# Optimization experiments

Measured on AMD Instinct MI355X. Metric: run time of the kernel, lower is better.

Reference implementation:

```python
import jax, jax.numpy as jnp
import numpy as np

N = 50000      # nodes
E = 640000     # edges
D_IN = 128     # input_dimension
H = 128        # hidden_dimension
D_OUT = 64     # output_dimension
G = 500        # num graphs
L = 2          # gnn layers (conv->norm->act stages each)
TEMP = 1.0     # mic_archi_param_temperature
EPS = 1e-5


def setup_inputs() -> dict:
    key = jax.random.key(0)
    ks = jax.random.split(key, 20)
    s = 1.0 / np.sqrt(H)
    inp = {
        "x": jax.random.normal(ks[0], (N, D_IN), jnp.float32),
        "edge_index": jax.random.randint(ks[1], (2, E), 0, N, dtype=jnp.int64),
        "batch": jnp.sort(jax.random.randint(ks[2], (N,), 0, G, dtype=jnp.int64)),
        # pre/post process MLPs (single Linear each)
        "pre_w": jax.random.normal(ks[3], (D_IN, H), jnp.float32) * s,
        "pre_b": jnp.zeros((H,), jnp.float32),
        "post_w": jax.random.normal(ks[4], (H, D_OUT), jnp.float32) * s,
        "post_b": jnp.zeros((D_OUT,), jnp.float32),
        # per-layer conv candidates: GCNConv + SAGEConv (stacked over L layers)
        "gcn_w": jax.random.normal(ks[5], (L, H, H), jnp.float32) * s,
        "gcn_b": jnp.zeros((L, H), jnp.float32),
        "sage_ws": jax.random.normal(ks[6], (L, H, H), jnp.float32) * s,
        "sage_wn": jax.random.normal(ks[7], (L, H, H), jnp.float32) * s,
        # per-layer norm candidate params (LayerNorm; Identity has none)
        "ln_g": jnp.ones((L, H), jnp.float32),
        "ln_b": jnp.zeros((L, H), jnp.float32),
        # architecture parameters (uniform init as in the torch code)
        "a_conv": jax.random.uniform(ks[8], (L, 2), jnp.float32),
        "a_norm": jax.random.uniform(ks[9], (L, 2), jnp.float32),
        "a_act": jax.random.uniform(ks[10], (L, 3), jnp.float32),
    }
    return inp


def reference(x, edge_index, batch, pre_w, pre_b, post_w, post_b,
              gcn_w, gcn_b, sage_ws, sage_wn, ln_g, ln_b,
              a_conv, a_norm, a_act):
    src, dst = edge_index[0], edge_index[1]
    loop = jnp.arange(N, dtype=src.dtype)
    # GCN uses self-loops + symmetric normalization
    src_sl = jnp.concatenate([src, loop])
    dst_sl = jnp.concatenate([dst, loop])
    deg = jax.ops.segment_sum(jnp.ones((E + N,), jnp.float32), dst_sl, num_segments=N)
    dinv = jax.lax.rsqrt(deg)  # deg >= 1 due to self-loops
    gcn_norm = (dinv[src_sl] * dinv[dst_sl])[:, None]  # [E+N, 1]
    # SAGE mean aggregation (no self loops)
    deg_n = jnp.clip(jax.ops.segment_sum(jnp.ones((E,), jnp.float32), dst, num_segments=N), 1.0)

    def gcn(h, w, b):
        hw = h @ w  # [N, H]
        agg = jax.ops.segment_sum(hw[src_sl] * gcn_norm, dst_sl, num_segments=N)
        return agg + b

    def sage(h, ws, wn):
        mean = jax.ops.segment_sum(h[src], dst, num_segments=N) / deg_n[:, None]
        return h @ ws + mean @ wn

    def layernorm(h, g, b):
        mu = jnp.mean(h, axis=-1, keepdims=True)
        var = jnp.mean(jnp.square(h - mu), axis=-1, keepdims=True)
        return (h - mu) * jax.lax.rsqrt(var + EPS) * g + b

    h = x @ pre_w + pre_b  # pre-process MLP
    layer_outputs = []
    for l in range(L):
        wc = jax.nn.softmax(a_conv[l] / TEMP)
        h = wc[0] * gcn(h, gcn_w[l], gcn_b[l]) + wc[1] * sage(h, sage_ws[l], sage_wn[l])
        wn_ = jax.nn.softmax(a_norm[l] / TEMP)
        h = wn_[0] * layernorm(h, ln_g[l], ln_b[l]) + wn_[1] * h
        wa = jax.nn.softmax(a_act[l] / TEMP)
        h = wa[0] * jax.nn.relu(h) + wa[1] * jnp.tanh(h) + wa[2] * jax.nn.elu(h)
        layer_outputs.append(h)  # collected after each act stage (skip connections)

    skip = layer_outputs[0]
    for o in layer_outputs[1:]:
        skip = skip + o
    pooled = jax.ops.segment_sum(skip, batch, num_segments=G)  # sum pooling readout
    return pooled @ post_w + post_b
```

## Files before the change

### kernel.cpp

```cpp
#include <hip/hip_runtime.h>
#include <hip/hip_fp16.h>
#include <math.h>

#define N_NODES 50000
#define N_EDGES 640000
#define HDIM    128
#define D_OUT   64
#define G_GRAPHS 500
#define EPSV    1e-5f
#define WPM     16384
#define CAP     64
#define SENT    N_NODES
#define NSHARD  8
#define SHARD_SZ ((N_NODES + NSHARD - 1) / NSHARD)

typedef __bf16 v8bf __attribute__((ext_vector_type(8)));
typedef float  f32x4 __attribute__((ext_vector_type(4)));

static __device__ __forceinline__ float bf_lo(unsigned u) {
    union { unsigned x; float f; } c; c.x = u << 16; return c.f;
}
static __device__ __forceinline__ float bf_hi(unsigned u) {
    union { unsigned x; float f; } c; c.x = u & 0xffff0000u; return c.f;
}

__global__ void setup_kernel(const float* __restrict__ pre_w,
                             const float* __restrict__ gcn_w,
                             const float* __restrict__ sws,
                             const float* __restrict__ swn,
                             const float* __restrict__ a_conv,
                             __bf16* __restrict__ Wp,
                             int* __restrict__ cnt,
                             float* __restrict__ pooled,
                             uint4* __restrict__ csr4,
                             uint4* __restrict__ hrow0,
                             uint4* __restrict__ hrow1)
{
    int t = blockIdx.x * blockDim.x + threadIdx.x;
    const unsigned sv = ((unsigned)SENT << 16) | (unsigned)SENT;
    if (t < N_NODES * CAP / 8) csr4[t] = make_uint4(sv, sv, sv, sv);
    if (t < N_NODES) cnt[t] = 0;
    if (t < G_GRAPHS * 128) pooled[t] = 0.f;
    if (t < 16) {
        hrow0[t] = make_uint4(0, 0, 0, 0);
        hrow1[t] = make_uint4(0, 0, 0, 0);
    }
    if (t >= 7 * 2048) return;
    int m    = t >> 11;
    int r    = t & 2047;
    int lane = r & 63;
    int fb   = r >> 6;
    int kc   = fb >> 3;
    int cb   = fb & 7;
    const float* W = pre_w;
    float scale = 1.f;
    if (m > 0) {
        int type = (m - 1) >> 1;
        int l    = (m - 1) & 1;
        float c0 = a_conv[l * 2], c1 = a_conv[l * 2 + 1];
        float mx = fmaxf(c0, c1);
        float e0 = __expf(c0 - mx), e1 = __expf(c1 - mx);
        float wc0 = e0 / (e0 + e1);
        scale = (type == 0) ? wc0 : (1.f - wc0);
        W = (type == 0) ? gcn_w + (size_t)l * WPM
          : (type == 1) ? sws   + (size_t)l * WPM
                        : swn   + (size_t)l * WPM;
    }
    int k0  = kc * 32 + (lane >> 4) * 8;
    int col = cb * 16 + (lane & 15);
    __bf16* out = Wp + (size_t)m * WPM + ((size_t)fb * 64 + lane) * 8;
    #pragma unroll
    for (int i = 0; i < 8; i++)
        out[i] = (__bf16)(scale * W[(size_t)(k0 + i) * 128 + col]);
}

__global__ void csr_fill_kernel(const int* __restrict__ src, const int* __restrict__ dst,
                                int* __restrict__ cnt,
                                unsigned short* __restrict__ csr, int E) {
    int chunk = blockIdx.x >> 3;
    int shard = blockIdx.x & 7;
    int e = chunk * 256 + threadIdx.x;
    if (e >= E) return;
    int d = dst[e];
    if (d / SHARD_SZ != shard) return;
    int s = src[e];
    int pos = atomicAdd(&cnt[d], 1);
    csr[(d << 6) + pos] = (unsigned short)s;
}

__global__ void dinvh_kernel(const int* __restrict__ cnt, __half* __restrict__ dinvh, int n) {
    int i = blockIdx.x * blockDim.x + threadIdx.x;
    if (i < n)  dinvh[i] = __float2half(rsqrtf((float)cnt[i] + 1.0f));
    if (i == n) dinvh[i] = __float2half(0.f);
}

__global__ __launch_bounds__(256) void fused_gather_bf16(
    const __bf16* __restrict__ hb,
    const unsigned short* __restrict__ csr,
    const int* __restrict__ cnt,
    const __half* __restrict__ dinvh,
    __bf16* __restrict__ aggGb,
    __bf16* __restrict__ meanb, int n)
{
    int w = threadIdx.x >> 6;
    int lane = threadIdx.x & 63;
    int d = blockIdx.x * 4 + w;
    if (d >= n) return;
    int c = cnt[d];
    float cf = (float)c;
    float did = rsqrtf(cf + 1.0f);
    float rd  = 1.0f / fmaxf(cf, 1.0f);
    int base = d << 6;
    int iters = (c + 15) >> 4;
    int q  = lane >> 4;
    int c8 = (lane & 15) * 8;

    float aG[8] = {0, 0, 0, 0, 0, 0, 0, 0};
    float aS[8] = {0, 0, 0, 0, 0, 0, 0, 0};

    for (int p = 0; p < iters; p++) {
        int s[4];
        #pragma unroll
        for (int k = 0; k < 4; k++)
            s[k] = csr[base + p * 16 + 4 * k + q];
        uint4 u[4];
        float ds[4];
        #pragma unroll
        for (int k = 0; k < 4; k++) {
            u[k]  = *(const uint4*)(hb + (size_t)s[k] * 128 + c8);
            ds[k] = __half2float(dinvh[s[k]]);
        }
        #pragma unroll
        for (int k = 0; k < 4; k++) {
            float wk = ds[k] * did;
            float v[8] = { bf_lo(u[k].x), bf_hi(u[k].x), bf_lo(u[k].y), bf_hi(u[k].y),
                           bf_lo(u[k].z), bf_hi(u[k].z), bf_lo(u[k].w), bf_hi(u[k].w) };
            #pragma unroll
            for (int j = 0; j < 8; j++) {
                aG[j] = fmaf(v[j], wk, aG[j]);
                aS[j] += v[j];
            }
        }
    }
    #pragma unroll
    for (int j = 0; j < 8; j++) {
        aG[j] += __shfl_xor(aG[j], 16);
        aG[j] += __shfl_xor(aG[j], 32);
        aS[j] += __shfl_xor(aS[j], 16);
        aS[j] += __shfl_xor(aS[j], 32);
    }
    if (q == 0) {
        uint4 ud = *(const uint4*)(hb + (size_t)d * 128 + c8);
        float vd[8] = { bf_lo(ud.x), bf_hi(ud.x), bf_lo(ud.y), bf_hi(ud.y),
                        bf_lo(ud.z), bf_hi(ud.z), bf_lo(ud.w), bf_hi(ud.w) };
        float sl = did * did;
        union { __bf16 b[8]; uint4 u; } pg, pm;
        #pragma unroll
        for (int j = 0; j < 8; j++) {
            pg.b[j] = (__bf16)fmaf(vd[j], sl, aG[j]);
            pm.b[j] = (__bf16)(aS[j] * rd);
        }
        *(uint4*)(aggGb + (size_t)d * 128 + c8) = pg.u;
        *(uint4*)(meanb + (size_t)d * 128 + c8) = pm.u;
    }
}

__global__ __launch_bounds__(256) void pre_gemm_mfma(
    const float* __restrict__ x, const __bf16* __restrict__ Wp0,
    const float* __restrict__ pre_b, __bf16* __restrict__ hb, int n)
{
    __shared__ __bf16 wlds[WPM];
    const int tid  = threadIdx.x;
    const int w    = tid >> 6;
    const int lane = tid & 63;
    const int r0 = blockIdx.x * 64 + w * 16;
    int rl = r0 + (lane & 15);
    if (rl >= n) rl = n - 1;
    const int kg = lane >> 4;

    {
        uint4* lds4 = (uint4*)wlds;
        const uint4* g = (const uint4*)Wp0;
        #pragma unroll
        for (int it = 0; it < 8; it++)
            lds4[it * 256 + tid] = g[it * 256 + tid];
    }

    f32x4 acc[8];
    #pragma unroll
    for (int cb = 0; cb < 8; cb++) acc[cb] = (f32x4)(0.f);

    v8bf af[4];
    #pragma unroll
    for (int kc = 0; kc < 4; kc++) {
        const float* ap = x + (size_t)rl * 128 + kc * 32 + kg * 8;
        float4 a0 = *(const float4*)ap;
        float4 a1 = *(const float4*)(ap + 4);
        v8bf v;
        v[0] = (__bf16)a0.x; v[1] = (__bf16)a0.y;
        v[2] = (__bf16)a0.z; v[3] = (__bf16)a0.w;
        v[4] = (__bf16)a1.x; v[5] = (__bf16)a1.y;
        v[6] = (__bf16)a1.z; v[7] = (__bf16)a1.w;
        af[kc] = v;
    }
    __syncthreads();

    #pragma unroll
    for (int kc = 0; kc < 4; kc++) {
        #pragma unroll
        for (int cb = 0; cb < 8; cb++) {
            int bo = ((kc * 8 + cb) * 64 + lane) * 8;
            acc[cb] = __builtin_amdgcn_mfma_f32_16x16x32_bf16(
                af[kc], *(const v8bf*)&wlds[bo], acc[cb], 0, 0, 0);
        }
    }
    int cl = lane & 15;
    #pragma unroll
    for (int cb = 0; cb < 8; cb++) {
        float bias = pre_b[cb * 16 + cl];
        #pragma unroll
        for (int j = 0; j < 4; j++) {
            int r = r0 + kg * 4 + j;
            if (r < n) hb[(size_t)r * 128 + cb * 16 + cl] = (__bf16)(acc[cb][j] + bias);
        }
    }
}

__global__ __launch_bounds__(256, 3) void layer_gemm_kernel(
    const __bf16* __restrict__ aggGb, const __bf16* __restrict__ hin,
    const __bf16* __restrict__ meanb,
    const __bf16* __restrict__ WpG, const __bf16* __restrict__ WpS,
    const __bf16* __restrict__ WpN,
    const float* __restrict__ gcn_b,
    const float* __restrict__ lng, const float* __restrict__ lnb,
    const float* __restrict__ anorm, const float* __restrict__ aact,
    const float* __restrict__ aconv,
    __bf16* __restrict__ hout, int n)
{
    __shared__ __bf16 wlds[3 * 16 * 64 * 8];
    const int tid  = threadIdx.x;
    const int w    = tid >> 6;
    const int lane = tid & 63;
    const int r0 = blockIdx.x * 64 + w * 16;
    int rl = r0 + (lane & 15);
    if (rl >= n) rl = n - 1;
    const int kg = lane >> 4;

    v8bf af[12];
    #pragma unroll
    for (int kc = 0; kc < 4; kc++) {
        size_t ao = (size_t)rl * 128 + kc * 32 + kg * 8;
        af[kc]     = *(const v8bf*)(aggGb + ao);
        af[4 + kc] = *(const v8bf*)(hin   + ao);
        af[8 + kc] = *(const v8bf*)(meanb + ao);
    }

    f32x4 acc[8];
    #pragma unroll
    for (int cb = 0; cb < 8; cb++) acc[cb] = (f32x4)(0.f);

    uint4* lds4 = (uint4*)wlds;

    {
        const uint4* gG = (const uint4*)WpG;
        const uint4* gS = (const uint4*)WpS;
        const uint4* gN = (const uint4*)WpN;
        #pragma unroll
        for (int it = 0; it < 12; it++) {
            int idx = it * 256 + tid;
            int m = idx >> 10;
            int r = idx & 1023;
            const uint4* g = (m == 0) ? gG : (m == 1) ? gS : gN;
            lds4[idx] = g[r];
        }
    }
    __syncthreads();
    #pragma unroll
    for (int kc2 = 0; kc2 < 2; kc2++) {
        #pragma unroll
        for (int cb = 0; cb < 8; cb++) {
            int bo = ((kc2 * 8 + cb) * 64 + lane) * 8;
            acc[cb] = __builtin_amdgcn_mfma_f32_16x16x32_bf16(
                af[kc2], *(const v8bf*)&wlds[bo], acc[cb], 0, 0, 0);
            acc[cb] = __builtin_amdgcn_mfma_f32_16x16x32_bf16(
                af[4 + kc2], *(const v8bf*)&wlds[8192 + bo], acc[cb], 0, 0, 0);
            acc[cb] = __builtin_amdgcn_mfma_f32_16x16x32_bf16(
                af[8 + kc2], *(const v8bf*)&wlds[16384 + bo], acc[cb], 0, 0, 0);
        }
    }
    __syncthreads();

    {
        const uint4* gG = (const uint4*)WpG + 1024;
        const uint4* gS = (const uint4*)WpS + 1024;
        const uint4* gN = (const uint4*)WpN + 1024;
        #pragma unroll
        for (int it = 0; it < 12; it++) {
            int idx = it * 256 + tid;
            int m = idx >> 10;
            int r = idx & 1023;
            const uint4* g = (m == 0) ? gG : (m == 1) ? gS : gN;
            lds4[idx] = g[r];
        }
    }
    __syncthreads();
    #pragma unroll
    for (int kc2 = 0; kc2 < 2; kc2++) {
        #pragma unroll
        for (int cb = 0; cb < 8; cb++) {
            int bo = ((kc2 * 8 + cb) * 64 + lane) * 8;
            acc[cb] = __builtin_amdgcn_mfma_f32_16x16x32_bf16(
                af[2 + kc2], *(const v8bf*)&wlds[bo], acc[cb], 0, 0, 0);
            acc[cb] = __builtin_amdgcn_mfma_f32_16x16x32_bf16(
                af[6 + kc2], *(const v8bf*)&wlds[8192 + bo], acc[cb], 0, 0, 0);
            acc[cb] = __builtin_amdgcn_mfma_f32_16x16x32_bf16(
                af[10 + kc2], *(const v8bf*)&wlds[16384 + bo], acc[cb], 0, 0, 0);
        }
    }

    float c0 = aconv[0], c1 = aconv[1];
    float m = fmaxf(c0, c1);
    float e0 = __expf(c0 - m), e1 = __expf(c1 - m);
    float wc0 = e0 / (e0 + e1);
    float q0 = anorm[0], q1 = anorm[1];
    m = fmaxf(q0, q1);
    e0 = __expf(q0 - m); e1 = __expf(q1 - m);
    float wn0 = e0 / (e0 + e1), wn1 = 1.f - wn0;
    float a0 = aact[0], a1 = aact[1], a2 = aact[2];
    m = fmaxf(fmaxf(a0, a1), a2);
    float f0 = __expf(a0 - m), f1 = __expf(a1 - m), f2 = __expf(a2 - m);
    float fs = 1.f / (f0 + f1 + f2);
    float wa0 = f0 * fs, wa1 = f1 * fs, wa2 = f2 * fs;

    int cl = lane & 15;
    float gbF[8], lg[8], lb[8];
    #pragma unroll
    for (int cb = 0; cb < 8; cb++) {
        int c = cb * 16 + cl;
        gbF[cb] = wc0 * gcn_b[c]; lg[cb] = lng[c]; lb[cb] = lnb[c];
    }

    float s[4] = {0, 0, 0, 0}, s2[4] = {0, 0, 0, 0};
    #pragma unroll
    for (int cb = 0; cb < 8; cb++)
        #pragma unroll
        for (int j = 0; j < 4; j++) {
            float tv = acc[cb][j] + gbF[cb];
            acc[cb][j] = tv;
            s[j] += tv;
            s2[j] = fmaf(tv, tv, s2[j]);
        }
    #pragma unroll
    for (int o = 1; o < 16; o <<= 1)
        #pragma unroll
        for (int j = 0; j < 4; j++) {
            s[j]  += __shfl_xor(s[j], o);
            s2[j] += __shfl_xor(s2[j], o);
        }
    float mu[4], rs[4];
    #pragma unroll
    for (int j = 0; j < 4; j++) {
        mu[j] = s[j] * (1.f / 128.f);
        float var = s2[j] * (1.f / 128.f) - mu[j] * mu[j];
        rs[j] = rsqrtf(var + EPSV);
    }

    #pragma unroll
    for (int j = 0; j < 4; j++) {
        int r = r0 + kg * 4 + j;
        if (r >= n) continue;
        #pragma unroll
        for (int cb = 0; cb < 8; cb++) {
            float tv = acc[cb][j];
            float ln = (tv - mu[j]) * rs[j] * lg[cb] + lb[cb];
            float hv = wn0 * ln + wn1 * tv;
            float rl_ = fmaxf(hv, 0.f);
            float ex2 = __expf(2.f * hv);
            float th = 1.f - 2.f * __builtin_amdgcn_rcpf(ex2 + 1.f);
            float el = hv > 0.f ? hv : __expf(hv) - 1.f;
            float out = wa0 * rl_ + wa1 * th + wa2 * el;
            hout[(size_t)r * 128 + cb * 16 + cl] = (__bf16)out;
        }
    }
}

__global__ __launch_bounds__(256) void pool_sum_kernel(
    const __bf16* __restrict__ h1, const __bf16* __restrict__ h2,
    const int* __restrict__ batch, float* __restrict__ pooled, int n)
{
    int c2  = (threadIdx.x & 63) * 2;
    int seg = threadIdx.x >> 6;
    int n0  = blockIdx.x * 128 + seg * 32;
    int g_cur = -1;
    float acc0 = 0.f, acc1 = 0.f;
    for (int i = 0; i < 32; i++) {
        int node = n0 + i;
        if (node >= n) break;
        int g = batch[node];
        if (g != g_cur) {
            if (g_cur >= 0) {
                atomicAdd(&pooled[(size_t)g_cur * 128 + c2], acc0);
                atomicAdd(&pooled[(size_t)g_cur * 128 + c2 + 1], acc1);
            }
            g_cur = g; acc0 = 0.f; acc1 = 0.f;
        }
        unsigned u1 = *(const unsigned*)(h1 + (size_t)node * 128 + c2);
        unsigned u2 = *(const unsigned*)(h2 + (size_t)node * 128 + c2);
        acc0 += bf_lo(u1) + bf_lo(u2);
        acc1 += bf_hi(u1) + bf_hi(u2);
    }
    if (g_cur >= 0) {
        atomicAdd(&pooled[(size_t)g_cur * 128 + c2], acc0);
        atomicAdd(&pooled[(size_t)g_cur * 128 + c2 + 1], acc1);
    }
}

__global__ __launch_bounds__(64) void post_gemm_kernel(
    const float* __restrict__ pooled, const float* __restrict__ W,
    const float* __restrict__ b, float* __restrict__ out)
{
    __shared__ float p_s[128];
    int g = blockIdx.x;
    int j = threadIdx.x;
    p_s[j]      = pooled[(size_t)g * 128 + j];
    p_s[j + 64] = pooled[(size_t)g * 128 + 64 + j];
    __syncthreads();
    float acc = b[j];
    #pragma unroll
    for (int k = 0; k < 128; k++)
        acc = fmaf(p_s[k], W[k * 64 + j], acc);
    out[(size_t)g * 64 + j] = acc;
}

extern "C" void kernel_launch(void* const* d_in, const int* in_sizes, int n_in,
                              void* d_out, int out_size, void* d_ws, size_t ws_size,
                              hipStream_t stream)
{
    const float* x       = (const float*)d_in[0];
    const int*   ei      = (const int*)d_in[1];
    const int*   batch   = (const int*)d_in[2];
    const float* pre_w   = (const float*)d_in[3];
    const float* pre_b   = (const float*)d_in[4];
    const float* post_w  = (const float*)d_in[5];
    const float* post_b  = (const float*)d_in[6];
    const float* gcn_w   = (const float*)d_in[7];
    const float* gcn_b   = (const float*)d_in[8];
    const float* sage_ws = (const float*)d_in[9];
    const float* sage_wn = (const float*)d_in[10];
    const float* ln_g    = (const float*)d_in[11];
    const float* ln_b    = (const float*)d_in[12];
    const float* a_conv  = (const float*)d_in[13];
    const float* a_norm  = (const float*)d_in[14];
    const float* a_act   = (const float*)d_in[15];

    const int* src = ei;
    const int* dst = ei + N_EDGES;

    char* wsp = (char*)d_ws;
    size_t off = 0;
    auto alloc = [&](size_t bytes) {
        char* p = wsp + off;
        off += (bytes + 255) & ~(size_t)255;
        return p;
    };
    const size_t NHB = (size_t)(N_NODES + 1) * 128 * sizeof(__bf16);
    __bf16*         hb0    = (__bf16*)alloc(NHB);
    __bf16*         h1b    = (__bf16*)alloc(NHB);
    __bf16*         h2b    = (__bf16*)alloc(NHB);
    __bf16*         aggGb  = (__bf16*)alloc(NHB);
    __bf16*         meanb  = (__bf16*)alloc(NHB);
    __bf16*         Wp     = (__bf16*)alloc((size_t)7 * WPM * sizeof(__bf16));
    __half*         dinvh  = (__half*)alloc((N_NODES + 1) * sizeof(__half));
    int*            cnt    = (int*)alloc(N_NODES * sizeof(int));
    unsigned short* csr    = (unsigned short*)alloc((size_t)N_NODES * CAP * sizeof(unsigned short));
    float*          pooled = (float*)alloc((size_t)G_GRAPHS * 128 * sizeof(float));

    const int GEMM_BLOCKS = (N_NODES + 63) / 64;
    const int GATHER_BLOCKS = (N_NODES + 3) / 4;
    const int SETUP_BLOCKS = (N_NODES * CAP / 8 + 255) / 256;
    const int FILL_BLOCKS  = ((N_EDGES + 255) / 256) * NSHARD;

    setup_kernel<<<SETUP_BLOCKS, 256, 0, stream>>>(
        pre_w, gcn_w, sage_ws, sage_wn, a_conv, Wp, cnt, pooled,
        (uint4*)csr,
        (uint4*)(hb0 + (size_t)N_NODES * 128),
        (uint4*)(h1b + (size_t)N_NODES * 128));

    csr_fill_kernel<<<FILL_BLOCKS, 256, 0, stream>>>(
        src, dst, cnt, csr, N_EDGES);
    dinvh_kernel<<<(N_NODES + 256) / 256, 256, 0, stream>>>(cnt, dinvh, N_NODES);

    pre_gemm_mfma<<<GEMM_BLOCKS, 256, 0, stream>>>(x, Wp, pre_b, hb0, N_NODES);

    const __bf16* hin[2]  = { hb0, h1b };
    __bf16*       hout[2] = { h1b, h2b };
    for (int l = 0; l < 2; l++) {
        fused_gather_bf16<<<GATHER_BLOCKS, 256, 0, stream>>>(
            hin[l], csr, cnt, dinvh, aggGb, meanb, N_NODES);
        layer_gemm_kernel<<<GEMM_BLOCKS, 256, 0, stream>>>(
            aggGb, hin[l], meanb,
            Wp + (size_t)(1 + l) * WPM, Wp + (size_t)(3 + l) * WPM, Wp + (size_t)(5 + l) * WPM,
            gcn_b + l * 128, ln_g + l * 128, ln_b + l * 128,
            a_norm + l * 2, a_act + l * 3, a_conv + l * 2,
            hout[l], N_NODES);
    }

    pool_sum_kernel<<<(N_NODES + 127) / 128, 256, 0, stream>>>(h1b, h2b, batch, pooled, N_NODES);
    post_gemm_kernel<<<G_GRAPHS, 64, 0, stream>>>(pooled, post_w, post_b, (float*)d_out);
}
```

Before: 175.6 us.

## Drop CSR sentinel fill and dinv kernel; use 512-thread layer GEMM blocks

Stops pre-filling the whole 50000x64 CSR array with sentinels. The gather now handles the partial last group of 16 with explicit bounds masking to the sentinel row, and computes dinv on the fly from cnt, which gets one extra zeroed slot for the sentinel. This removes a large memset-style write and a separate kernel launch, at the cost of an extra cnt lookup per neighbor. It also doubles the layer GEMM block to 512 threads and 128 rows, halving the weight staging per row, with launch bounds changed to (512,4).

```diff
diff --git a/kernel.cpp b/kernel.cpp
--- a/kernel.cpp
+++ b/kernel.cpp
@@ -32,14 +32,11 @@
                              __bf16* __restrict__ Wp,
                              int* __restrict__ cnt,
                              float* __restrict__ pooled,
-                             uint4* __restrict__ csr4,
                              uint4* __restrict__ hrow0,
                              uint4* __restrict__ hrow1)
 {
     int t = blockIdx.x * blockDim.x + threadIdx.x;
-    const unsigned sv = ((unsigned)SENT << 16) | (unsigned)SENT;
-    if (t < N_NODES * CAP / 8) csr4[t] = make_uint4(sv, sv, sv, sv);
-    if (t < N_NODES) cnt[t] = 0;
+    if (t <= N_NODES) cnt[t] = 0;
     if (t < G_GRAPHS * 128) pooled[t] = 0.f;
     if (t < 16) {
         hrow0[t] = make_uint4(0, 0, 0, 0);
@@ -88,17 +85,10 @@
     csr[(d << 6) + pos] = (unsigned short)s;
 }
 
-__global__ void dinvh_kernel(const int* __restrict__ cnt, __half* __restrict__ dinvh, int n) {
-    int i = blockIdx.x * blockDim.x + threadIdx.x;
-    if (i < n)  dinvh[i] = __float2half(rsqrtf((float)cnt[i] + 1.0f));
-    if (i == n) dinvh[i] = __float2half(0.f);
-}
-
 __global__ __launch_bounds__(256) void fused_gather_bf16(
     const __bf16* __restrict__ hb,
     const unsigned short* __restrict__ csr,
     const int* __restrict__ cnt,
-    const __half* __restrict__ dinvh,
     __bf16* __restrict__ aggGb,
     __bf16* __restrict__ meanb, int n)
 {
@@ -111,14 +101,14 @@
     float did = rsqrtf(cf + 1.0f);
     float rd  = 1.0f / fmaxf(cf, 1.0f);
     int base = d << 6;
-    int iters = (c + 15) >> 4;
+    int full = c >> 4;
     int q  = lane >> 4;
     int c8 = (lane & 15) * 8;
 
     float aG[8] = {0, 0, 0, 0, 0, 0, 0, 0};
     float aS[8] = {0, 0, 0, 0, 0, 0, 0, 0};
 
-    for (int p = 0; p < iters; p++) {
+    for (int p = 0; p < full; p++) {
         int s[4];
         #pragma unroll
         for (int k = 0; k < 4; k++)
@@ -128,7 +118,33 @@
         #pragma unroll
         for (int k = 0; k < 4; k++) {
             u[k]  = *(const uint4*)(hb + (size_t)s[k] * 128 + c8);
-            ds[k] = __half2float(dinvh[s[k]]);
+            ds[k] = rsqrtf((float)cnt[s[k]] + 1.0f);
+        }
+        #pragma unroll
+        for (int k = 0; k < 4; k++) {
+            float wk = ds[k] * did;
+            float v[8] = { bf_lo(u[k].x), bf_hi(u[k].x), bf_lo(u[k].y), bf_hi(u[k].y),
+                           bf_lo(u[k].z), bf_hi(u[k].z), bf_lo(u[k].w), bf_hi(u[k].w) };
+            #pragma unroll
+            for (int j = 0; j < 8; j++) {
+                aG[j] = fmaf(v[j], wk, aG[j]);
+                aS[j] += v[j];
+            }
+        }
+    }
+    if (c & 15) {
+        int s[4];
+        #pragma unroll
+        for (int k = 0; k < 4; k++) {
+            int idx = full * 16 + 4 * k + q;
+            s[k] = (idx < c) ? (int)csr[base + idx] : SENT;
+        }
+        uint4 u[4];
+        float ds[4];
+        #pragma unroll
+        for (int k = 0; k < 4; k++) {
+            u[k]  = *(const uint4*)(hb + (size_t)s[k] * 128 + c8);
+            ds[k] = rsqrtf((float)cnt[s[k]] + 1.0f);
         }
         #pragma unroll
         for (int k = 0; k < 4; k++) {
@@ -226,7 +242,7 @@
     }
 }
 
-__global__ __launch_bounds__(256, 3) void layer_gemm_kernel(
+__global__ __launch_bounds__(512, 4) void layer_gemm_kernel(
     const __bf16* __restrict__ aggGb, const __bf16* __restrict__ hin,
     const __bf16* __restrict__ meanb,
     const __bf16* __restrict__ WpG, const __bf16* __restrict__ WpS,
@@ -241,7 +257,7 @@
     const int tid  = threadIdx.x;
     const int w    = tid >> 6;
     const int lane = tid & 63;
-    const int r0 = blockIdx.x * 64 + w * 16;
+    const int r0 = blockIdx.x * 128 + w * 16;
     int rl = r0 + (lane & 15);
     if (rl >= n) rl = n - 1;
     const int kg = lane >> 4;
@@ -266,8 +282,8 @@
         const uint4* gS = (const uint4*)WpS;
         const uint4* gN = (const uint4*)WpN;
         #pragma unroll
-        for (int it = 0; it < 12; it++) {
-            int idx = it * 256 + tid;
+        for (int it = 0; it < 6; it++) {
+            int idx = it * 512 + tid;
             int m = idx >> 10;
             int r = idx & 1023;
             const uint4* g = (m == 0) ? gG : (m == 1) ? gS : gN;
@@ -295,8 +311,8 @@
         const uint4* gS = (const uint4*)WpS + 1024;
         const uint4* gN = (const uint4*)WpN + 1024;
         #pragma unroll
-        for (int it = 0; it < 12; it++) {
-            int idx = it * 256 + tid;
+        for (int it = 0; it < 6; it++) {
+            int idx = it * 512 + tid;
             int m = idx >> 10;
             int r = idx & 1023;
             const uint4* g = (m == 0) ? gG : (m == 1) ? gS : gN;
@@ -470,34 +486,32 @@
     __bf16*         aggGb  = (__bf16*)alloc(NHB);
     __bf16*         meanb  = (__bf16*)alloc(NHB);
     __bf16*         Wp     = (__bf16*)alloc((size_t)7 * WPM * sizeof(__bf16));
-    __half*         dinvh  = (__half*)alloc((N_NODES + 1) * sizeof(__half));
-    int*            cnt    = (int*)alloc(N_NODES * sizeof(int));
+    int*            cnt    = (int*)alloc((N_NODES + 1) * sizeof(int));
     unsigned short* csr    = (unsigned short*)alloc((size_t)N_NODES * CAP * sizeof(unsigned short));
     float*          pooled = (float*)alloc((size_t)G_GRAPHS * 128 * sizeof(float));
 
-    const int GEMM_BLOCKS = (N_NODES + 63) / 64;
+    const int PRE_BLOCKS   = (N_NODES + 63) / 64;
+    const int LAYER_BLOCKS = (N_NODES + 127) / 128;
     const int GATHER_BLOCKS = (N_NODES + 3) / 4;
-    const int SETUP_BLOCKS = (N_NODES * CAP / 8 + 255) / 256;
+    const int SETUP_BLOCKS = (G_GRAPHS * 128 + 255) / 256;
     const int FILL_BLOCKS  = ((N_EDGES + 255) / 256) * NSHARD;
 
     setup_kernel<<<SETUP_BLOCKS, 256, 0, stream>>>(
         pre_w, gcn_w, sage_ws, sage_wn, a_conv, Wp, cnt, pooled,
-        (uint4*)csr,
         (uint4*)(hb0 + (size_t)N_NODES * 128),
         (uint4*)(h1b + (size_t)N_NODES * 128));
 
     csr_fill_kernel<<<FILL_BLOCKS, 256, 0, stream>>>(
         src, dst, cnt, csr, N_EDGES);
-    dinvh_kernel<<<(N_NODES + 256) / 256, 256, 0, stream>>>(cnt, dinvh, N_NODES);
-
-    pre_gemm_mfma<<<GEMM_BLOCKS, 256, 0, stream>>>(x, Wp, pre_b, hb0, N_NODES);
+
+    pre_gemm_mfma<<<PRE_BLOCKS, 256, 0, stream>>>(x, Wp, pre_b, hb0, N_NODES);
 
     const __bf16* hin[2]  = { hb0, h1b };
     __bf16*       hout[2] = { h1b, h2b };
     for (int l = 0; l < 2; l++) {
         fused_gather_bf16<<<GATHER_BLOCKS, 256, 0, stream>>>(
-            hin[l], csr, cnt, dinvh, aggGb, meanb, N_NODES);
-        layer_gemm_kernel<<<GEMM_BLOCKS, 256, 0, stream>>>(
+            hin[l], csr, cnt, aggGb, meanb, N_NODES);
+        layer_gemm_kernel<<<LAYER_BLOCKS, 512, 0, stream>>>(
             aggGb, hin[l], meanb,
             Wp + (size_t)(1 + l) * WPM, Wp + (size_t)(3 + l) * WPM, Wp + (size_t)(5 + l) * WPM,
             gcn_b + l * 128, ln_g + l * 128, ln_b + l * 128,
```

Result: no change. 176.9 us (+0.7%).
